# Kernel tuning notes

Hardware: AMD Instinct MI355X
Metric: run time of the kernel (lower is better)

Reference implementation:

```python
import jax, jax.numpy as jnp
import numpy as np

N_USERS = 100000
N_ENTITIES = 100000
D = 64
NNZ = 3200000
N_HOPS = 3
EPS = 1e-12


def _l2_normalize(x):
    # F.normalize(dim=-1): x / max(||x||_2, eps)
    norm = jnp.sqrt(jnp.sum(x * x, axis=-1, keepdims=True))
    return x / jnp.maximum(norm, EPS)


def setup_inputs() -> dict:
    key = jax.random.key(0)
    k1, k2, k3, k4, k5 = jax.random.split(key, 5)
    user_emb = jax.random.normal(k1, (N_USERS, D), dtype=jnp.float32)
    entity_emb = jax.random.normal(k2, (N_ENTITIES, D), dtype=jnp.float32)
    edge_u = jax.random.randint(k3, (NNZ,), 0, N_USERS, dtype=jnp.int32)
    edge_e = jax.random.randint(k4, (NNZ,), 0, N_ENTITIES, dtype=jnp.int32)
    edge_w = jax.random.uniform(k5, (NNZ,), dtype=jnp.float32)
    return {"user_emb": user_emb, "entity_emb": entity_emb,
            "edge_u": edge_u, "edge_e": edge_e, "edge_w": edge_w}


def reference(user_emb, entity_emb, edge_u, edge_e, edge_w):
    # interact_mat: sparse [n_users, n_entities] in COO (edge_u, edge_e, edge_w).
    # Eval-mode forward (dropout identity), as used at inference.
    entity_res = entity_emb
    user_res = user_emb
    w = edge_w[:, None]  # [nnz, 1]
    for _ in range(N_HOPS):
        # entity_agg = interact_mat.T @ user_emb : scatter user rows into entities
        entity_agg = jax.ops.segment_sum(w * user_emb[edge_u], edge_e,
                                         num_segments=N_ENTITIES)
        # user_agg = interact_mat @ entity_emb : scatter entity rows into users
        user_agg = jax.ops.segment_sum(w * entity_emb[edge_e], edge_u,
                                       num_segments=N_USERS)
        entity_emb = _l2_normalize(entity_agg)
        user_emb = _l2_normalize(user_agg)
        entity_res = entity_res + entity_emb
        user_res = user_res + user_emb
    return (entity_res, user_res)
```

## Files before the change

### kernel.cpp

```cpp
#include <hip/hip_runtime.h>


#define NU     100000
#define NE     100000
#define DD     64
#define NNZ    3200000
#define NROWS  200000
#define EMB    6400000
#define TOT    6400000

#define SHIFT  9
#define RPB    512
#define NBUK   391
#define NBLK   512
#define TILE   (NNZ / NBLK)

__device__ __forceinline__ float bf2f(ushort v) {
    return __uint_as_float(((unsigned int)v) << 16);
}
__device__ __forceinline__ ushort f2bf(float x) {
    unsigned int b = __float_as_uint(x);
    return (ushort)((b + 0x7FFF + ((b >> 16) & 1)) >> 16);
}

__global__ void k_init(const float4* __restrict__ uemb,
                       const float4* __restrict__ eemb,
                       ushort4* __restrict__ ucur, ushort4* __restrict__ ecur,
                       float4* __restrict__ out) {
    const int n4 = EMB / 4;
    int tid = blockIdx.x * blockDim.x + threadIdx.x;
    int stride = gridDim.x * blockDim.x;
    for (int i = tid; i < n4; i += stride) {
        float4 u = uemb[i], e = eemb[i];
        ushort4 ub, eb;
        ub.x = f2bf(u.x); ub.y = f2bf(u.y); ub.z = f2bf(u.z); ub.w = f2bf(u.w);
        eb.x = f2bf(e.x); eb.y = f2bf(e.y); eb.z = f2bf(e.z); eb.w = f2bf(e.w);
        ucur[i] = ub;
        ecur[i] = eb;
        out[i]      = e;
        out[n4 + i] = u;
    }
}

__global__ void __launch_bounds__(256) k_bhist(const int* __restrict__ eu,
                                               const int* __restrict__ ee,
                                               int* __restrict__ pos) {
    __shared__ int h[NBUK];
    int t = threadIdx.x;
    for (int b = t; b < NBUK; b += 256) h[b] = 0;
    __syncthreads();
    int start = blockIdx.x * TILE, end = start + TILE;
    for (int i = start + t; i < end; i += 256) {
        atomicAdd(&h[ee[i] >> SHIFT], 1);
        atomicAdd(&h[(NE + eu[i]) >> SHIFT], 1);
    }
    __syncthreads();
    for (int b = t; b < NBUK; b += 256) pos[b * NBLK + blockIdx.x] = h[b];
}

__global__ void k_gsum(const int* __restrict__ a, int* __restrict__ partials, int n) {
    int gid = blockIdx.x * 256 + threadIdx.x;
    int v = (gid < n) ? a[gid] : 0;
    for (int d = 32; d; d >>= 1) v += __shfl_down(v, d);
    __shared__ int ws[4];
    if ((threadIdx.x & 63) == 0) ws[threadIdx.x >> 6] = v;
    __syncthreads();
    if (threadIdx.x == 0) partials[blockIdx.x] = ws[0] + ws[1] + ws[2] + ws[3];
}

__global__ void k_gtop(int* __restrict__ partials, int nb) {
    int tid = threadIdx.x;
    int v = (tid < nb) ? partials[tid] : 0;
    int lane = tid & 63, wid = tid >> 6;
    int x = v;
    for (int d = 1; d < 64; d <<= 1) { int tv = __shfl_up(x, d); if (lane >= d) x += tv; }
    __shared__ int wsum[16], woff[16];
    if (lane == 63) wsum[wid] = x;
    __syncthreads();
    if (tid < 16) {
        int s = 0;
        for (int i = 0; i < tid; i++) s += wsum[i];
        woff[tid] = s;
    }
    __syncthreads();
    int excl = x + woff[wid] - v;
    if (tid < nb) partials[tid] = excl;
}

__global__ void k_gfinal(int* __restrict__ a, const int* __restrict__ partials, int n) {
    int gid = blockIdx.x * 256 + threadIdx.x;
    int v = (gid < n) ? a[gid] : 0;
    int lane = threadIdx.x & 63, wid = threadIdx.x >> 6;
    int x = v;
    for (int d = 1; d < 64; d <<= 1) { int tv = __shfl_up(x, d); if (lane >= d) x += tv; }
    __shared__ int ws[4];
    if (lane == 63) ws[wid] = x;
    __syncthreads();
    int add = 0;
    for (int i = 0; i < wid; i++) add += ws[i];
    int excl = x - v + add + partials[blockIdx.x];
    if (gid < n) a[gid] = excl;
}

__global__ void __launch_bounds__(256) k_partB(const int* __restrict__ eu,
                                               const int* __restrict__ ee,
                                               const float* __restrict__ ew,
                                               const int* __restrict__ pos,
                                               int2* __restrict__ recs) {
    __shared__ int cur[NBUK];
    int t = threadIdx.x;
    for (int b = t; b < NBUK; b += 256) cur[b] = pos[b * NBLK + blockIdx.x];
    __syncthreads();
    int start = blockIdx.x * TILE, end = start + TILE;
    for (int i = start + t; i < end; i += 256) {
        int u = eu[i], e = ee[i];
        int wb = __float_as_int(ew[i]);
        int r1 = e;
        int p1 = atomicAdd(&cur[r1 >> SHIFT], 1);
        recs[p1] = make_int2(((r1 & (RPB - 1)) << 17) | u, wb);
        int r2 = NE + u;
        int p2 = atomicAdd(&cur[r2 >> SHIFT], 1);
        recs[p2] = make_int2(((r2 & (RPB - 1)) << 17) | e, wb);
    }
}

__global__ void __launch_bounds__(256) k_partC(const int* __restrict__ pos,
                                               const int2* __restrict__ recs,
                                               int2* __restrict__ edges,
                                               int* __restrict__ row_ptr) {
    int b = blockIdx.x;
    int t = threadIdx.x;
    __shared__ int hist[RPB];
    __shared__ int curs[RPB];
    __shared__ int wtot[4];
    int base = pos[b * NBLK];
    int nend = (b == NBUK - 1) ? TOT : pos[(b + 1) * NBLK];
    for (int r = t; r < RPB; r += 256) hist[r] = 0;
    __syncthreads();
    for (int i = base + t; i < nend; i += 256)
        atomicAdd(&hist[recs[i].x >> 17], 1);
    __syncthreads();
    int h0 = hist[2 * t], h1 = hist[2 * t + 1];
    int s = h0 + h1;
    int lane = t & 63, wid = t >> 6;
    int x = s;
    for (int d = 1; d < 64; d <<= 1) { int v = __shfl_up(x, d); if (lane >= d) x += v; }
    if (lane == 63) wtot[wid] = x;
    __syncthreads();
    int woff = 0;
    for (int i = 0; i < wid; i++) woff += wtot[i];
    int e0 = base + woff + x - s;
    curs[2 * t]     = e0;
    curs[2 * t + 1] = e0 + h0;
    int row0 = (b << SHIFT) + 2 * t;
    if (row0 < NROWS)     row_ptr[row0]     = e0;
    if (row0 + 1 < NROWS) row_ptr[row0 + 1] = e0 + h0;
    if (b == 0 && t == 0) row_ptr[NROWS]    = TOT;
    __syncthreads();
    for (int i = base + t; i < nend; i += 256) {
        int2 rc = recs[i];
        int p = atomicAdd(&curs[rc.x >> 17], 1);
        edges[p] = make_int2(rc.x & 0x1FFFF, rc.y);
    }
}

__global__ void __launch_bounds__(256) k_agg(
        const int* __restrict__ row_ptr, const int2* __restrict__ edges,
        const ushort* __restrict__ uold, const ushort* __restrict__ eold,
        ushort* __restrict__ unew, ushort* __restrict__ enew,
        float* __restrict__ out) {
    int wid = threadIdx.x >> 6;
    int row = __builtin_amdgcn_readfirstlane(blockIdx.x * 4 + wid);
    if (row >= NROWS) return;
    int lane = threadIdx.x & 63;

    const ushort* __restrict__ src;
    ushort* dst; float* op;
    if (row < NE) {
        src = uold;
        dst = enew + (size_t)row * DD;
        op  = out  + (size_t)row * DD;
    } else {
        int r = row - NE;
        src = eold;
        dst = unew + (size_t)r * DD;
        op  = out + EMB + (size_t)r * DD;
    }

    int s = row_ptr[row], e = row_ptr[row + 1];
    float acc = 0.f;
    int j = s;
    for (; j + 4 <= e; j += 4) {
        int2 c0 = edges[j];
        int2 c1 = edges[j + 1];
        int2 c2 = edges[j + 2];
        int2 c3 = edges[j + 3];
        float g0 = bf2f(src[c0.x * DD + lane]);
        float g1 = bf2f(src[c1.x * DD + lane]);
        float g2 = bf2f(src[c2.x * DD + lane]);
        float g3 = bf2f(src[c3.x * DD + lane]);
        acc = fmaf(__int_as_float(c0.y), g0, acc);
        acc = fmaf(__int_as_float(c1.y), g1, acc);
        acc = fmaf(__int_as_float(c2.y), g2, acc);
        acc = fmaf(__int_as_float(c3.y), g3, acc);
    }
    for (; j < e; j++) {
        int2 c = edges[j];
        acc = fmaf(__int_as_float(c.y), bf2f(src[c.x * DD + lane]), acc);
    }

    float sq = acc * acc;
    for (int d = 32; d; d >>= 1) sq += __shfl_xor(sq, d);
    float nv = acc / fmaxf(sqrtf(sq), 1e-12f);

    dst[lane] = f2bf(nv);
    op[lane] += nv;
}

extern "C" void kernel_launch(void* const* d_in, const int* in_sizes, int n_in,
                              void* d_out, int out_size, void* d_ws, size_t ws_size,
                              hipStream_t stream) {
    const float* uemb = (const float*)d_in[0];
    const float* eemb = (const float*)d_in[1];
    const int*   eu   = (const int*)d_in[2];
    const int*   ee   = (const int*)d_in[3];
    const float* ew   = (const float*)d_in[4];
    float* out = (float*)d_out;

    char* ws = (char*)d_ws;
    size_t off = 0;
    ushort* ucur0 = (ushort*)(ws + off); off += (size_t)EMB * 2;
    ushort* ecur0 = (ushort*)(ws + off); off += (size_t)EMB * 2;
    ushort* ucur1 = (ushort*)(ws + off); off += (size_t)EMB * 2;
    ushort* ecur1 = (ushort*)(ws + off); off += (size_t)EMB * 2;
    int2*  recs    = (int2*)(ws + off);  off += (size_t)TOT * 8;
    int2*  edges   = (int2*)(ws + off);  off += (size_t)TOT * 8;
    int*   row_ptr = (int*)(ws + off);   off += (size_t)(NROWS + 1) * 4;
    int*   pos     = (int*)(ws + off);   off += (size_t)NBUK * NBLK * 4;
    int*   partials= (int*)(ws + off);   off += 1024 * 4;

    k_init<<<2048, 256, 0, stream>>>((const float4*)uemb, (const float4*)eemb,
                                     (ushort4*)ucur0, (ushort4*)ecur0, (float4*)out);

    k_bhist<<<NBLK, 256, 0, stream>>>(eu, ee, pos);

    const int NSCAN = NBUK * NBLK;
    const int NB = (NSCAN + 255) / 256;
    k_gsum<<<NB, 256, 0, stream>>>(pos, partials, NSCAN);
    k_gtop<<<1, 1024, 0, stream>>>(partials, NB);
    k_gfinal<<<NB, 256, 0, stream>>>(pos, partials, NSCAN);

    k_partB<<<NBLK, 256, 0, stream>>>(eu, ee, ew, pos, recs);

    k_partC<<<NBUK, 256, 0, stream>>>(pos, recs, edges, row_ptr);

    const int AB = (NROWS + 3) / 4;
    k_agg<<<AB, 256, 0, stream>>>(row_ptr, edges, ucur0, ecur0, ucur1, ecur1, out);
    k_agg<<<AB, 256, 0, stream>>>(row_ptr, edges, ucur1, ecur1, ucur0, ecur0, out);
    k_agg<<<AB, 256, 0, stream>>>(row_ptr, edges, ucur0, ecur0, ucur1, ecur1, out);
}
```

Before: 801.4 us.

## Split wavefront into four edge slots with 8-byte vector gathers in aggregation

The aggregation kernel now splits each 64-lane wavefront into four 16-lane slots. Each slot processes a different edge and each lane loads 4 bf16 values (uint2), so one wavefront covers four edges per gather instruction instead of one. Partial sums are combined with cross-slot shuffles, then normalized, with packed f32x2 FMAs used for the math. This raises memory-level parallelism and reduces the instruction count per edge, at the cost of extra shuffle reductions and masked tail handling.

```diff
diff --git a/kernel.cpp b/kernel.cpp
--- a/kernel.cpp
+++ b/kernel.cpp
@@ -14,6 +14,8 @@
 #define NBUK   391
 #define NBLK   512
 #define TILE   (NNZ / NBLK)
+
+typedef float f32x2 __attribute__((ext_vector_type(2)));
 
 __device__ __forceinline__ float bf2f(ushort v) {
     return __uint_as_float(((unsigned int)v) << 16);
@@ -173,48 +175,99 @@
     int row = __builtin_amdgcn_readfirstlane(blockIdx.x * 4 + wid);
     if (row >= NROWS) return;
     int lane = threadIdx.x & 63;
-
-    const ushort* __restrict__ src;
+    int slot = lane >> 4;
+    int l15  = lane & 15;
+
+    const uint2* __restrict__ src;
     ushort* dst; float* op;
     if (row < NE) {
-        src = uold;
+        src = (const uint2*)uold;
         dst = enew + (size_t)row * DD;
         op  = out  + (size_t)row * DD;
     } else {
         int r = row - NE;
-        src = eold;
+        src = (const uint2*)eold;
         dst = unew + (size_t)r * DD;
         op  = out + EMB + (size_t)r * DD;
     }
 
     int s = row_ptr[row], e = row_ptr[row + 1];
-    float acc = 0.f;
+    f32x2 a0 = {0.f, 0.f};
+    f32x2 a1 = {0.f, 0.f};
+
     int j = s;
+    for (; j + 16 <= e; j += 16) {
+        int2 rA = edges[j      + slot];
+        int2 rB = edges[j + 4  + slot];
+        int2 rC = edges[j + 8  + slot];
+        int2 rD = edges[j + 12 + slot];
+        uint2 gA = src[rA.x * 16 + l15];
+        uint2 gB = src[rB.x * 16 + l15];
+        uint2 gC = src[rC.x * 16 + l15];
+        uint2 gD = src[rD.x * 16 + l15];
+        f32x2 wA = {__int_as_float(rA.y), __int_as_float(rA.y)};
+        f32x2 wB = {__int_as_float(rB.y), __int_as_float(rB.y)};
+        f32x2 wC = {__int_as_float(rC.y), __int_as_float(rC.y)};
+        f32x2 wD = {__int_as_float(rD.y), __int_as_float(rD.y)};
+        f32x2 pA0 = {__uint_as_float(gA.x << 16), __uint_as_float(gA.x & 0xFFFF0000u)};
+        f32x2 pA1 = {__uint_as_float(gA.y << 16), __uint_as_float(gA.y & 0xFFFF0000u)};
+        f32x2 pB0 = {__uint_as_float(gB.x << 16), __uint_as_float(gB.x & 0xFFFF0000u)};
+        f32x2 pB1 = {__uint_as_float(gB.y << 16), __uint_as_float(gB.y & 0xFFFF0000u)};
+        f32x2 pC0 = {__uint_as_float(gC.x << 16), __uint_as_float(gC.x & 0xFFFF0000u)};
+        f32x2 pC1 = {__uint_as_float(gC.y << 16), __uint_as_float(gC.y & 0xFFFF0000u)};
+        f32x2 pD0 = {__uint_as_float(gD.x << 16), __uint_as_float(gD.x & 0xFFFF0000u)};
+        f32x2 pD1 = {__uint_as_float(gD.y << 16), __uint_as_float(gD.y & 0xFFFF0000u)};
+        a0 = pA0 * wA + a0;  a1 = pA1 * wA + a1;
+        a0 = pB0 * wB + a0;  a1 = pB1 * wB + a1;
+        a0 = pC0 * wC + a0;  a1 = pC1 * wC + a1;
+        a0 = pD0 * wD + a0;  a1 = pD1 * wD + a1;
+    }
     for (; j + 4 <= e; j += 4) {
-        int2 c0 = edges[j];
-        int2 c1 = edges[j + 1];
-        int2 c2 = edges[j + 2];
-        int2 c3 = edges[j + 3];
-        float g0 = bf2f(src[c0.x * DD + lane]);
-        float g1 = bf2f(src[c1.x * DD + lane]);
-        float g2 = bf2f(src[c2.x * DD + lane]);
-        float g3 = bf2f(src[c3.x * DD + lane]);
-        acc = fmaf(__int_as_float(c0.y), g0, acc);
-        acc = fmaf(__int_as_float(c1.y), g1, acc);
-        acc = fmaf(__int_as_float(c2.y), g2, acc);
-        acc = fmaf(__int_as_float(c3.y), g3, acc);
-    }
-    for (; j < e; j++) {
-        int2 c = edges[j];
-        acc = fmaf(__int_as_float(c.y), bf2f(src[c.x * DD + lane]), acc);
-    }
-
-    float sq = acc * acc;
-    for (int d = 32; d; d >>= 1) sq += __shfl_xor(sq, d);
-    float nv = acc / fmaxf(sqrtf(sq), 1e-12f);
-
-    dst[lane] = f2bf(nv);
-    op[lane] += nv;
+        int2 r = edges[j + slot];
+        uint2 g = src[r.x * 16 + l15];
+        f32x2 w = {__int_as_float(r.y), __int_as_float(r.y)};
+        f32x2 p0 = {__uint_as_float(g.x << 16), __uint_as_float(g.x & 0xFFFF0000u)};
+        f32x2 p1 = {__uint_as_float(g.y << 16), __uint_as_float(g.y & 0xFFFF0000u)};
+        a0 = p0 * w + a0;
+        a1 = p1 * w + a1;
+    }
+    if (j < e) {
+        int idx = j + slot;
+        bool valid = idx < e;
+        int2 r = edges[valid ? idx : (e - 1)];
+        uint2 g = src[r.x * 16 + l15];
+        float wf = valid ? __int_as_float(r.y) : 0.f;
+        f32x2 w = {wf, wf};
+        f32x2 p0 = {__uint_as_float(g.x << 16), __uint_as_float(g.x & 0xFFFF0000u)};
+        f32x2 p1 = {__uint_as_float(g.y << 16), __uint_as_float(g.y & 0xFFFF0000u)};
+        a0 = p0 * w + a0;
+        a1 = p1 * w + a1;
+    }
+
+    a0.x += __shfl_xor(a0.x, 16); a0.y += __shfl_xor(a0.y, 16);
+    a1.x += __shfl_xor(a1.x, 16); a1.y += __shfl_xor(a1.y, 16);
+    a0.x += __shfl_xor(a0.x, 32); a0.y += __shfl_xor(a0.y, 32);
+    a1.x += __shfl_xor(a1.x, 32); a1.y += __shfl_xor(a1.y, 32);
+
+    float sq = a0.x * a0.x;
+    sq = fmaf(a0.y, a0.y, sq);
+    sq = fmaf(a1.x, a1.x, sq);
+    sq = fmaf(a1.y, a1.y, sq);
+    for (int d = 8; d; d >>= 1) sq += __shfl_xor(sq, d);
+    float inv = 1.0f / fmaxf(sqrtf(sq), 1e-12f);
+    float n0 = a0.x * inv, n1 = a0.y * inv, n2 = a1.x * inv, n3 = a1.y * inv;
+
+    if (slot == 0) {
+        uint2 p;
+        p.x = (uint)f2bf(n0) | ((uint)f2bf(n1) << 16);
+        p.y = (uint)f2bf(n2) | ((uint)f2bf(n3) << 16);
+        ((uint2*)dst)[l15] = p;
+    } else if (slot == 1) {
+        float4* o4 = (float4*)op;
+        float4 c = o4[l15];
+        c.x += n0; c.y += n1; c.z += n2; c.w += n3;
+        o4[l15] = c;
+    }
 }
 
 extern "C" void kernel_launch(void* const* d_in, const int* in_sizes, int n_in,
```

Measured after the change: 720.9 us. 10.0% less time.
